# Kernel optimization log

Hardware: AMD Instinct MI355X
Metric: run time of the kernel (lower is better)

Reference implementation:

```python
import jax, jax.numpy as jnp
import numpy as np

B, L, DIM = 2, 2048, 1024
H, DH, W = 16, 64, 256  # heads, head_dim, window_size
ROPE_BASE = 10000.0


def _rope(x):
    # x: [b, l, h, d] -> rotate consecutive pairs (torch view_as_complex semantics)
    l, d = x.shape[1], x.shape[3]
    freqs = 1.0 / (ROPE_BASE ** (jnp.arange(0, d, 2, dtype=jnp.float32) / d))  # [d/2]
    ang = jnp.arange(l, dtype=jnp.float32)[:, None] * freqs[None, :]           # [l, d/2]
    cos = jnp.cos(ang)[None, :, None, :].astype(x.dtype)
    sin = jnp.sin(ang)[None, :, None, :].astype(x.dtype)
    xe, xo = x[..., 0::2], x[..., 1::2]
    ye = xe * cos - xo * sin
    yo = xe * sin + xo * cos
    return jnp.stack([ye, yo], axis=-1).reshape(x.shape)


def setup_inputs() -> dict:
    key = jax.random.key(0)
    ks = jax.random.split(key, 7)
    sh = (B, L, DIM)
    return {
        "q": jax.random.normal(ks[0], sh, jnp.float32),
        "k": jax.random.normal(ks[1], sh, jnp.float32),
        "v": jax.random.normal(ks[2], sh, jnp.float32),
        "wq": jax.random.normal(ks[3], (H * DH, DIM), jnp.float32) * 0.02,
        "wk": jax.random.normal(ks[4], (H * DH, DIM), jnp.float32) * 0.02,
        "wv": jax.random.normal(ks[5], (H * DH, DIM), jnp.float32) * 0.02,
        "wo": jax.random.normal(ks[6], (DIM, H * DH), jnp.float32) * 0.02,
    }


def reference(q, k, v, wq, wk, wv, wo):
    b, l, _ = q.shape
    qh = (q @ wq.T).reshape(b, l, H, DH)
    kh = (k @ wk.T).reshape(b, l, H, DH)
    vh = (v @ wv.T).reshape(b, l, H, DH).transpose(0, 2, 1, 3)  # [b,h,l,d]
    qh = _rope(qh).transpose(0, 2, 1, 3)                        # [b,h,l,d]
    kh = _rope(kh).transpose(0, 2, 1, 3)
    scores = jnp.einsum('bhqd,bhkd->bhqk', qh, kh) * (DH ** -0.5)
    i = jnp.arange(l)[:, None]
    j = jnp.arange(l)[None, :]
    window_mask = (j <= i) & (j >= i - W)  # keys in [i-W, i], matches the loop
    scores = jnp.where(window_mask, scores, -1e30)
    probs = jax.nn.softmax(scores, axis=-1)
    out = jnp.einsum('bhqk,bhkd->bhqd', probs, vh)
    out = out.transpose(0, 2, 1, 3).reshape(b, l, H * DH)
    return out @ wo.T
```

## Files before the change

### kernel.cpp

```cpp
#include <hip/hip_runtime.h>
#include <stdint.h>

#define B_    2
#define L_    2048
#define DIM_  1024
#define H_    16
#define DH_   64
#define WWIN  256

typedef __attribute__((ext_vector_type(4))) float f32x4;
typedef __attribute__((ext_vector_type(8))) short bf16x8;

__device__ __forceinline__ unsigned short f2bf(float x) {
  union { float f; unsigned u; } c; c.f = x;
  unsigned r = c.u + 0x7fffu + ((c.u >> 16) & 1u);
  return (unsigned short)(r >> 16);
}
__device__ __forceinline__ float bf2f(unsigned short u) {
  union { unsigned u; float f; } c; c.u = ((unsigned)u) << 16; return c.f;
}

struct CastArgs {
  const float* src[7];
  unsigned short* dst[7];
  int n[7];
};
__global__ __launch_bounds__(256) void cast_bf16_kernel(CastArgs a) {
  int arr = blockIdx.y;
  int i = (blockIdx.x * 256 + threadIdx.x) * 4;
  if (i >= a.n[arr]) return;
  float4 v = *(const float4*)(a.src[arr] + i);
  ushort4 o;
  o.x = f2bf(v.x); o.y = f2bf(v.y); o.z = f2bf(v.z); o.w = f2bf(v.w);
  *(ushort4*)(a.dst[arr] + i) = o;
}

#define BM 128
#define BN 128
#define BK 64

__device__ __forceinline__ void gld_lds16(const void* g, void* l) {
  __builtin_amdgcn_global_load_lds(
      (const __attribute__((address_space(1))) void*)g,
      (__attribute__((address_space(3))) void*)l, 16, 0, 0);
}

__device__ __forceinline__ void gemm_core_1024(
    const unsigned short* __restrict__ A, const unsigned short* __restrict__ Bt,
    unsigned short* As, unsigned short* Bs, f32x4 (&acc)[4][4]) {
  const int tid = threadIdx.x;
  const int wave = tid >> 6, lane = tid & 63;
  const int quad = lane >> 4, l16 = lane & 15;
  const int wm = wave >> 1, wn = wave & 1;
  const int m0 = blockIdx.y * BM, n0 = blockIdx.x * BN;
  const int srow = tid >> 3, sc = tid & 7;

  for (int k0 = 0; k0 < 1024; k0 += BK) {
    #pragma unroll
    for (int rd = 0; rd < 4; ++rd) {
      int row = rd * 32 + srow;
      int cs = sc ^ (row & 7);
      gld_lds16(A + (size_t)(m0 + row) * 1024 + k0 + cs * 8, As + (size_t)row * BK + sc * 8);
      gld_lds16(Bt + (size_t)(n0 + row) * 1024 + k0 + cs * 8, Bs + (size_t)row * BK + sc * 8);
    }
    __syncthreads();
    #pragma unroll
    for (int ks = 0; ks < 2; ++ks) {
      bf16x8 af[4], bfr[4];
      #pragma unroll
      for (int i = 0; i < 4; ++i) {
        int row = wm * 64 + i * 16 + l16;
        int ch = (ks * 4 + quad) ^ (row & 7);
        af[i] = *(const bf16x8*)(As + row * BK + ch * 8);
      }
      #pragma unroll
      for (int j = 0; j < 4; ++j) {
        int row = wn * 64 + j * 16 + l16;
        int ch = (ks * 4 + quad) ^ (row & 7);
        bfr[j] = *(const bf16x8*)(Bs + row * BK + ch * 8);
      }
      #pragma unroll
      for (int i = 0; i < 4; ++i)
        #pragma unroll
        for (int j = 0; j < 4; ++j)
          acc[i][j] = __builtin_amdgcn_mfma_f32_16x16x32_bf16(af[i], bfr[j], acc[i][j], 0, 0, 0);
    }
    __syncthreads();
  }
}

struct ProjArgs {
  const unsigned short* A[3];
  const unsigned short* Bt[3];
  unsigned short* C[3];
};
__global__ __launch_bounds__(256) void gemm_proj_kernel(ProjArgs pa) {
  __shared__ unsigned short As[BM * BK];
  __shared__ unsigned short Bs[BN * BK];
  const int z = blockIdx.z;
  f32x4 acc[4][4] = {};
  gemm_core_1024(pa.A[z], pa.Bt[z], As, Bs, acc);

  const int lane = threadIdx.x & 63, wave = threadIdx.x >> 6;
  const int quad = lane >> 4, l16 = lane & 15;
  const int wm = wave >> 1, wn = wave & 1;
  const int m0 = blockIdx.y * BM, n0 = blockIdx.x * BN;
  unsigned short* C = pa.C[z];
  #pragma unroll
  for (int i = 0; i < 4; ++i)
    #pragma unroll
    for (int j = 0; j < 4; ++j)
      #pragma unroll
      for (int r = 0; r < 4; ++r) {
        int m = m0 + wm * 64 + i * 16 + quad * 4 + r;
        int n = n0 + wn * 64 + j * 16 + l16;
        int b = m >> 11, l = m & (L_ - 1);
        int h = n >> 6, d = n & 63;
        C[(((size_t)b * H_ + h) * L_ + l) * DH_ + d] = f2bf(acc[i][j][r]);
      }
}

__global__ __launch_bounds__(256) void gemm_out_kernel(
    const unsigned short* __restrict__ A, const unsigned short* __restrict__ Bt,
    float* __restrict__ C) {
  __shared__ unsigned short As[BM * BK];
  __shared__ unsigned short Bs[BN * BK];
  f32x4 acc[4][4] = {};
  gemm_core_1024(A, Bt, As, Bs, acc);

  const int lane = threadIdx.x & 63, wave = threadIdx.x >> 6;
  const int quad = lane >> 4, l16 = lane & 15;
  const int wm = wave >> 1, wn = wave & 1;
  const int m0 = blockIdx.y * BM, n0 = blockIdx.x * BN;
  #pragma unroll
  for (int i = 0; i < 4; ++i)
    #pragma unroll
    for (int j = 0; j < 4; ++j)
      #pragma unroll
      for (int r = 0; r < 4; ++r) {
        int m = m0 + wm * 64 + i * 16 + quad * 4 + r;
        int n = n0 + wn * 64 + j * 16 + l16;
        C[(size_t)m * DIM_ + n] = acc[i][j][r];
      }
}

__global__ __launch_bounds__(256) void rope_kernel(unsigned short* __restrict__ qh,
                                                   unsigned short* __restrict__ kh) {
  int idx = blockIdx.x * 256 + threadIdx.x;
  unsigned short* p = blockIdx.y ? kh : qh;
  int d2 = idx & 31;
  int l = (idx >> 5) & (L_ - 1);
  int bh = idx >> 16;
  size_t base = ((size_t)bh * L_ + l) * DH_ + d2 * 2;
  unsigned v = *(const unsigned*)(p + base);
  float xe = bf2f((unsigned short)(v & 0xffffu));
  float xo = bf2f((unsigned short)(v >> 16));
  float freq = exp2f(-(float)d2 * 0.41524101186092029f);
  float ang = (float)l * freq;
  float s, c;
  sincosf(ang, &s, &c);
  unsigned short ye = f2bf(xe * c - xo * s);
  unsigned short yo = f2bf(xe * s + xo * c);
  *(unsigned*)(p + base) = (unsigned)ye | ((unsigned)yo << 16);
}

__global__ __launch_bounds__(256) void transpose_v_kernel(const unsigned short* __restrict__ vh,
                                                          unsigned short* __restrict__ vt) {
  __shared__ unsigned short t[64 * 72];
  int bh = blockIdx.y, l0 = blockIdx.x * 64, tid = threadIdx.x;
  int r = tid >> 2, cg = tid & 3;
  #pragma unroll
  for (int rep = 0; rep < 2; ++rep) {
    int col = cg * 16 + rep * 8;
    *(uint4*)(&t[r * 72 + col]) =
        *(const uint4*)(vh + ((size_t)bh * L_ + l0 + r) * DH_ + col);
  }
  __syncthreads();
  #pragma unroll
  for (int rep = 0; rep < 2; ++rep) {
    int col = cg * 16 + rep * 8;
    unsigned short tmp[8];
    #pragma unroll
    for (int k2 = 0; k2 < 8; ++k2) tmp[k2] = t[(col + k2) * 72 + r];
    uint4 o;
    o.x = (unsigned)tmp[0] | ((unsigned)tmp[1] << 16);
    o.y = (unsigned)tmp[2] | ((unsigned)tmp[3] << 16);
    o.z = (unsigned)tmp[4] | ((unsigned)tmp[5] << 16);
    o.w = (unsigned)tmp[6] | ((unsigned)tmp[7] << 16);
    *(uint4*)(vt + ((size_t)bh * DH_ + r) * L_ + l0 + col) = o;
  }
}

#define NCH 20
__global__ __launch_bounds__(256) void attn_kernel(
    const unsigned short* __restrict__ Qh,
    const unsigned short* __restrict__ Kh,
    const unsigned short* __restrict__ Vt,
    unsigned short* __restrict__ O) {
  __shared__ unsigned short KVs[160 * 72];
  __shared__ unsigned short Ps[4][16 * 40];
  const int tid = threadIdx.x;
  const int wave = tid >> 6, lane = tid & 63;
  const int quad = lane >> 4, l16 = lane & 15;
  const int q0 = blockIdx.x * 64;
  const int bh = blockIdx.y;
  const int kwin0 = q0 - WWIN;
  const int qb = q0 + wave * 16;

  bf16x8 qf0, qf1;
  {
    const unsigned short* qrow = Qh + ((size_t)bh * L_ + qb + l16) * DH_;
    qf0 = *(const bf16x8*)(qrow + quad * 8);
    qf1 = *(const bf16x8*)(qrow + 32 + quad * 8);
  }

  f32x4 S[NCH] = {};

  #pragma unroll
  for (int half = 0; half < 2; ++half) {
    __syncthreads();
    for (int rep = 0; rep < 5; ++rep) {
      int ci = rep * 256 + tid;
      int row = ci >> 3, c = ci & 7;
      int key = kwin0 + half * 160 + row;
      uint4 val = {0, 0, 0, 0};
      if (key >= 0)
        val = *(const uint4*)(Kh + ((size_t)bh * L_ + key) * DH_ + c * 8);
      *(uint4*)(&KVs[row * 72 + c * 8]) = val;
    }
    __syncthreads();
    #pragma unroll
    for (int cc = 0; cc < 10; ++cc) {
      const unsigned short* kr = &KVs[(cc * 16 + l16) * 72];
      bf16x8 kf0 = *(const bf16x8*)(kr + quad * 8);
      bf16x8 kf1 = *(const bf16x8*)(kr + 32 + quad * 8);
      int c = half * 10 + cc;
      S[c] = __builtin_amdgcn_mfma_f32_16x16x32_bf16(qf0, kf0, S[c], 0, 0, 0);
      S[c] = __builtin_amdgcn_mfma_f32_16x16x32_bf16(qf1, kf1, S[c], 0, 0, 0);
    }
  }

  float inv_l[4];
  #pragma unroll
  for (int r = 0; r < 4; ++r) {
    int i = qb + quad * 4 + r;
    float mx = -1e30f;
    #pragma unroll
    for (int c = 0; c < NCH; ++c) {
      int key = kwin0 + c * 16 + l16;
      bool valid = (key >= 0) && (key <= i) && (key >= i - WWIN);
      float v = valid ? S[c][r] * 0.125f : -1e30f;
      S[c][r] = v;
      mx = fmaxf(mx, v);
    }
    mx = fmaxf(mx, __shfl_xor(mx, 1));
    mx = fmaxf(mx, __shfl_xor(mx, 2));
    mx = fmaxf(mx, __shfl_xor(mx, 4));
    mx = fmaxf(mx, __shfl_xor(mx, 8));
    float sum = 0.f;
    #pragma unroll
    for (int c = 0; c < NCH; ++c) {
      float e = __expf(S[c][r] - mx);
      S[c][r] = e;
      sum += e;
    }
    sum += __shfl_xor(sum, 1);
    sum += __shfl_xor(sum, 2);
    sum += __shfl_xor(sum, 4);
    sum += __shfl_xor(sum, 8);
    inv_l[r] = 1.0f / sum;
  }

  f32x4 Oacc[4] = {};
  #pragma unroll
  for (int half = 0; half < 2; ++half) {
    __syncthreads();
    for (int rep = 0; rep < 5; ++rep) {
      int ci = rep * 256 + tid;
      int row = ci / 20, c = ci % 20;
      int key0 = kwin0 + half * 160 + c * 8;
      uint4 val = {0, 0, 0, 0};
      if (key0 >= 0)
        val = *(const uint4*)(Vt + ((size_t)bh * DH_ + row) * L_ + key0);
      *(uint4*)(&KVs[row * 168 + c * 8]) = val;
    }
    __syncthreads();
    #pragma unroll
    for (int s = 0; s < 5; ++s) {
      int cbase = half * 10 + s * 2;
      unsigned short* pw = &Ps[wave][0];
      #pragma unroll
      for (int cc = 0; cc < 2; ++cc)
        #pragma unroll
        for (int r = 0; r < 4; ++r) {
          float p = S[cbase + cc][r] * inv_l[r];
          pw[(quad * 4 + r) * 40 + cc * 16 + l16] = f2bf(p);
        }
      asm volatile("s_waitcnt lgkmcnt(0)" ::: "memory");
      bf16x8 pf = *(const bf16x8*)(pw + l16 * 40 + quad * 8);
      int lk = s * 32 + quad * 8;
      #pragma unroll
      for (int t = 0; t < 4; ++t) {
        bf16x8 vf = *(const bf16x8*)(&KVs[(t * 16 + l16) * 168 + lk]);
        Oacc[t] = __builtin_amdgcn_mfma_f32_16x16x32_bf16(pf, vf, Oacc[t], 0, 0, 0);
      }
    }
  }

  int b = bh >> 4, h = bh & 15;
  #pragma unroll
  for (int t = 0; t < 4; ++t)
    #pragma unroll
    for (int r = 0; r < 4; ++r) {
      int l = qb + quad * 4 + r;
      int col = h * DH_ + t * 16 + l16;
      O[((size_t)b * L_ + l) * (H_ * DH_) + col] = f2bf(Oacc[t][r]);
    }
}

extern "C" void kernel_launch(void* const* d_in, const int* in_sizes, int n_in,
                              void* d_out, int out_size, void* d_ws, size_t ws_size,
                              hipStream_t stream) {
  const float* q  = (const float*)d_in[0];
  const float* k  = (const float*)d_in[1];
  const float* v  = (const float*)d_in[2];
  const float* wq = (const float*)d_in[3];
  const float* wk = (const float*)d_in[4];
  const float* wv = (const float*)d_in[5];
  const float* wo = (const float*)d_in[6];

  const size_t SA = (size_t)B_ * L_ * DIM_;
  const size_t SW = (size_t)DIM_ * DIM_;
  unsigned short* w   = (unsigned short*)d_ws;
  unsigned short* qb  = w; w += SA;
  unsigned short* kb  = w; w += SA;
  unsigned short* vb  = w; w += SA;
  unsigned short* wqb = w; w += SW;
  unsigned short* wkb = w; w += SW;
  unsigned short* wvb = w; w += SW;
  unsigned short* wob = w; w += SW;
  unsigned short* qh  = w; w += SA;
  unsigned short* kh  = w; w += SA;
  unsigned short* vh  = w; w += SA;
  unsigned short* vt  = w; w += SA;
  unsigned short* Ob  = w; w += SA;

  CastArgs ca;
  ca.src[0] = q;  ca.dst[0] = qb;  ca.n[0] = (int)SA;
  ca.src[1] = k;  ca.dst[1] = kb;  ca.n[1] = (int)SA;
  ca.src[2] = v;  ca.dst[2] = vb;  ca.n[2] = (int)SA;
  ca.src[3] = wq; ca.dst[3] = wqb; ca.n[3] = (int)SW;
  ca.src[4] = wk; ca.dst[4] = wkb; ca.n[4] = (int)SW;
  ca.src[5] = wv; ca.dst[5] = wvb; ca.n[5] = (int)SW;
  ca.src[6] = wo; ca.dst[6] = wob; ca.n[6] = (int)SW;
  cast_bf16_kernel<<<dim3(SA / (256 * 4), 7), 256, 0, stream>>>(ca);

  ProjArgs pa;
  pa.A[0] = qb; pa.Bt[0] = wqb; pa.C[0] = qh;
  pa.A[1] = kb; pa.Bt[1] = wkb; pa.C[1] = kh;
  pa.A[2] = vb; pa.Bt[2] = wvb; pa.C[2] = vh;
  gemm_proj_kernel<<<dim3(DIM_ / BN, (B_ * L_) / BM, 3), 256, 0, stream>>>(pa);

  rope_kernel<<<dim3((B_ * H_ * L_ * DH_ / 2) / 256, 2), 256, 0, stream>>>(qh, kh);
  transpose_v_kernel<<<dim3(L_ / 64, B_ * H_), 256, 0, stream>>>(vh, vt);
  attn_kernel<<<dim3(L_ / 64, B_ * H_), 256, 0, stream>>>(qh, kh, vt, Ob);
  gemm_out_kernel<<<dim3(DIM_ / BN, (B_ * L_) / BM), 256, 0, stream>>>(Ob, wob, (float*)d_out);
}
```

Before: 216.3 us.

## Fuse RoPE and V transpose into projection GEMM epilogue

Applies rotary embedding to Q/K directly in the projection GEMM epilogue, using lane-pair shuffles and hardware sin/cos on a range-reduced angle. For V, the epilogue stages the tile through XOR-swizzled shared memory and writes it transposed. This removes the separate rope and transpose kernels along with their global memory round trips. The trade-off is more epilogue work, and the hardware sin/cos has lower accuracy than sincosf.

```diff
diff --git a/kernel.cpp b/kernel.cpp
--- a/kernel.cpp
+++ b/kernel.cpp
@@ -15,9 +15,6 @@
   union { float f; unsigned u; } c; c.f = x;
   unsigned r = c.u + 0x7fffu + ((c.u >> 16) & 1u);
   return (unsigned short)(r >> 16);
-}
-__device__ __forceinline__ float bf2f(unsigned short u) {
-  union { unsigned u; float f; } c; c.u = ((unsigned)u) << 16; return c.f;
 }
 
 struct CastArgs {
@@ -95,29 +92,78 @@
   unsigned short* C[3];
 };
 __global__ __launch_bounds__(256) void gemm_proj_kernel(ProjArgs pa) {
-  __shared__ unsigned short As[BM * BK];
-  __shared__ unsigned short Bs[BN * BK];
+  __shared__ unsigned short SH[16384];
+  unsigned short* As = SH;
+  unsigned short* Bs = SH + 8192;
   const int z = blockIdx.z;
   f32x4 acc[4][4] = {};
   gemm_core_1024(pa.A[z], pa.Bt[z], As, Bs, acc);
 
-  const int lane = threadIdx.x & 63, wave = threadIdx.x >> 6;
+  const int tid = threadIdx.x;
+  const int lane = tid & 63, wave = tid >> 6;
   const int quad = lane >> 4, l16 = lane & 15;
   const int wm = wave >> 1, wn = wave & 1;
   const int m0 = blockIdx.y * BM, n0 = blockIdx.x * BN;
-  unsigned short* C = pa.C[z];
-  #pragma unroll
-  for (int i = 0; i < 4; ++i)
-    #pragma unroll
-    for (int j = 0; j < 4; ++j)
+
+  if (z < 2) {
+    float frev[4];
+    #pragma unroll
+    for (int j = 0; j < 4; ++j) {
+      int d = (wn * 64 + j * 16 + l16) & 63;
+      frev[j] = exp2f(-(float)(d >> 1) * 0.41524101186092029f) * 0.15915494309189535f;
+    }
+    unsigned short* C = pa.C[z];
+    const bool even = (l16 & 1) == 0;
+    #pragma unroll
+    for (int i = 0; i < 4; ++i)
       #pragma unroll
       for (int r = 0; r < 4; ++r) {
         int m = m0 + wm * 64 + i * 16 + quad * 4 + r;
-        int n = n0 + wn * 64 + j * 16 + l16;
         int b = m >> 11, l = m & (L_ - 1);
-        int h = n >> 6, d = n & 63;
-        C[(((size_t)b * H_ + h) * L_ + l) * DH_ + d] = f2bf(acc[i][j][r]);
-      }
+        float lf = (float)l;
+        #pragma unroll
+        for (int j = 0; j < 4; ++j) {
+          int ng = n0 + wn * 64 + j * 16 + l16;
+          int h = (ng >> 6) & 15, d = ng & 63;
+          float v = acc[i][j][r];
+          float p = __shfl_xor(v, 1);
+          float a = lf * frev[j];
+          float t = a - floorf(a);
+          float s = __builtin_amdgcn_sinf(t);
+          float c = __builtin_amdgcn_cosf(t);
+          float o = even ? (v * c - p * s) : (p * s + v * c);
+          C[(((size_t)b * H_ + h) * L_ + l) * DH_ + d] = f2bf(o);
+        }
+      }
+  } else {
+    unsigned short* T = SH + wave * 4096;
+    #pragma unroll
+    for (int i = 0; i < 4; ++i)
+      #pragma unroll
+      for (int j = 0; j < 4; ++j) {
+        int nw = j * 16 + l16;
+        int hm = i * 4 + quad;
+        int off = nw * 64 + ((hm ^ (nw & 15)) << 2);
+        uint2 pk;
+        pk.x = (unsigned)f2bf(acc[i][j][0]) | ((unsigned)f2bf(acc[i][j][1]) << 16);
+        pk.y = (unsigned)f2bf(acc[i][j][2]) | ((unsigned)f2bf(acc[i][j][3]) << 16);
+        *(uint2*)(T + off) = pk;
+      }
+    asm volatile("s_waitcnt lgkmcnt(0)" ::: "memory");
+    int ng = n0 + wn * 64 + lane;
+    int h = (ng >> 6) & 15, d = ng & 63;
+    int b = m0 >> 11;
+    int lbase = (m0 & (L_ - 1)) + wm * 64;
+    unsigned short* C = pa.C[2];
+    size_t rowbase = (((size_t)b * H_ + h) * DH_ + d) * L_ + lbase;
+    #pragma unroll
+    for (int t = 0; t < 8; ++t) {
+      uint2 lo = *(uint2*)(T + lane * 64 + (((2 * t) ^ (lane & 15)) << 2));
+      uint2 hi = *(uint2*)(T + lane * 64 + (((2 * t + 1) ^ (lane & 15)) << 2));
+      uint4 o = {lo.x, lo.y, hi.x, hi.y};
+      *(uint4*)(C + rowbase + t * 8) = o;
+    }
+  }
 }
 
 __global__ __launch_bounds__(256) void gemm_out_kernel(
@@ -142,53 +188,6 @@
         int n = n0 + wn * 64 + j * 16 + l16;
         C[(size_t)m * DIM_ + n] = acc[i][j][r];
       }
-}
-
-__global__ __launch_bounds__(256) void rope_kernel(unsigned short* __restrict__ qh,
-                                                   unsigned short* __restrict__ kh) {
-  int idx = blockIdx.x * 256 + threadIdx.x;
-  unsigned short* p = blockIdx.y ? kh : qh;
-  int d2 = idx & 31;
-  int l = (idx >> 5) & (L_ - 1);
-  int bh = idx >> 16;
-  size_t base = ((size_t)bh * L_ + l) * DH_ + d2 * 2;
-  unsigned v = *(const unsigned*)(p + base);
-  float xe = bf2f((unsigned short)(v & 0xffffu));
-  float xo = bf2f((unsigned short)(v >> 16));
-  float freq = exp2f(-(float)d2 * 0.41524101186092029f);
-  float ang = (float)l * freq;
-  float s, c;
-  sincosf(ang, &s, &c);
-  unsigned short ye = f2bf(xe * c - xo * s);
-  unsigned short yo = f2bf(xe * s + xo * c);
-  *(unsigned*)(p + base) = (unsigned)ye | ((unsigned)yo << 16);
-}
-
-__global__ __launch_bounds__(256) void transpose_v_kernel(const unsigned short* __restrict__ vh,
-                                                          unsigned short* __restrict__ vt) {
-  __shared__ unsigned short t[64 * 72];
-  int bh = blockIdx.y, l0 = blockIdx.x * 64, tid = threadIdx.x;
-  int r = tid >> 2, cg = tid & 3;
-  #pragma unroll
-  for (int rep = 0; rep < 2; ++rep) {
-    int col = cg * 16 + rep * 8;
-    *(uint4*)(&t[r * 72 + col]) =
-        *(const uint4*)(vh + ((size_t)bh * L_ + l0 + r) * DH_ + col);
-  }
-  __syncthreads();
-  #pragma unroll
-  for (int rep = 0; rep < 2; ++rep) {
-    int col = cg * 16 + rep * 8;
-    unsigned short tmp[8];
-    #pragma unroll
-    for (int k2 = 0; k2 < 8; ++k2) tmp[k2] = t[(col + k2) * 72 + r];
-    uint4 o;
-    o.x = (unsigned)tmp[0] | ((unsigned)tmp[1] << 16);
-    o.y = (unsigned)tmp[2] | ((unsigned)tmp[3] << 16);
-    o.z = (unsigned)tmp[4] | ((unsigned)tmp[5] << 16);
-    o.w = (unsigned)tmp[6] | ((unsigned)tmp[7] << 16);
-    *(uint4*)(vt + ((size_t)bh * DH_ + r) * L_ + l0 + col) = o;
-  }
 }
 
 #define NCH 20
@@ -341,7 +340,6 @@
   unsigned short* wob = w; w += SW;
   unsigned short* qh  = w; w += SA;
   unsigned short* kh  = w; w += SA;
-  unsigned short* vh  = w; w += SA;
   unsigned short* vt  = w; w += SA;
   unsigned short* Ob  = w; w += SA;
 
@@ -358,11 +356,9 @@
   ProjArgs pa;
   pa.A[0] = qb; pa.Bt[0] = wqb; pa.C[0] = qh;
   pa.A[1] = kb; pa.Bt[1] = wkb; pa.C[1] = kh;
-  pa.A[2] = vb; pa.Bt[2] = wvb; pa.C[2] = vh;
+  pa.A[2] = vb; pa.Bt[2] = wvb; pa.C[2] = vt;
   gemm_proj_kernel<<<dim3(DIM_ / BN, (B_ * L_) / BM, 3), 256, 0, stream>>>(pa);
 
-  rope_kernel<<<dim3((B_ * H_ * L_ * DH_ / 2) / 256, 2), 256, 0, stream>>>(qh, kh);
-  transpose_v_kernel<<<dim3(L_ / 64, B_ * H_), 256, 0, stream>>>(vh, vt);
   attn_kernel<<<dim3(L_ / 64, B_ * H_), 256, 0, stream>>>(qh, kh, vt, Ob);
   gemm_out_kernel<<<dim3(DIM_ / BN, (B_ * L_) / BM), 256, 0, stream>>>(Ob, wob, (float*)d_out);
 }
```

New measurement: 213.6 us. About the same (-1.3%).
